# Performance work log

Measured on AMD Instinct MI355X. Metric: run time of the kernel, lower is better.

## Reference

```python
import jax, jax.numpy as jnp
import numpy as np

H = 512   # hidden_size
E = 256   # embedding_size
V = 32000 # vocab_size
L = 1024  # max_length (encoder seq len)
B = 64    # batch


def setup_inputs() -> dict:
    key = jax.random.key(0)
    ks = jax.random.split(key, 18)
    n = lambda i, shape, s=0.05: (jax.random.normal(ks[i], shape, dtype=jnp.float32) * s)
    return {
        "input": jax.random.randint(ks[0], (B, 1), 0, V),
        "last_output_context": n(1, (1, B, H), 1.0),
        "last_hidden": n(2, (1, B, H), 1.0),
        "last_cell_state": n(3, (1, B, H), 1.0),
        "encoder_outputs": n(4, (L, B, H), 1.0),
        "emb": n(5, (V, E)),
        "W_ih": n(6, (4 * H, E + H)),
        "W_hh": n(7, (4 * H, H)),
        "b_ih": n(8, (4 * H,)),
        "b_hh": n(9, (4 * H,)),
        "W_attn": n(10, (H, 2 * H)),
        "b_attn": n(11, (H,)),
        "beta": n(12, (H, 1), 1.0),
        "W_oc": n(13, (H, 2 * H)),
        "b_oc": n(14, (H,)),
        "W_out": n(15, (V, H)),
        "b_out": n(16, (V,)),
    }


def reference(input, last_output_context, last_hidden, last_cell_state,
              encoder_outputs, emb, W_ih, W_hh, b_ih, b_hh,
              W_attn, b_attn, beta, W_oc, b_oc, W_out, b_out):
    # embedding lookup: (B,1) -> (B,E)  (permute(1,0,2) then squeeze step dim)
    tok = emb[input[:, 0]]                                   # (B, E)
    x = jnp.concatenate([tok, last_output_context[0]], axis=1)  # (B, E+H)
    # single-step LSTM (PyTorch gate order i, f, g, o)
    gates = x @ W_ih.T + last_hidden[0] @ W_hh.T + b_ih + b_hh  # (B, 4H)
    i_g, f_g, g_g, o_g = jnp.split(gates, 4, axis=1)
    i_g = jax.nn.sigmoid(i_g)
    f_g = jax.nn.sigmoid(f_g)
    g_g = jnp.tanh(g_g)
    o_g = jax.nn.sigmoid(o_g)
    c = f_g * last_cell_state[0] + i_g * g_g                  # (B, H)
    h = o_g * jnp.tanh(c)                                     # (B, H) == rnn_output
    # additive attention, vectorized over the seq_len loop
    h_tiled = jnp.broadcast_to(h[None], (L, B, H))
    cat = jnp.concatenate([h_tiled, encoder_outputs], axis=-1)  # (L, B, 2H)
    energy = jnp.tanh(cat @ W_attn.T + b_attn) @ beta           # (L, B, 1)
    attn_w = jax.nn.softmax(energy[..., 0], axis=0)             # (L, B) softmax over seq
    # context = bmm(attn_weights, encoder_outputs)
    context = jnp.einsum('lb,lbh->bh', attn_w, encoder_outputs)  # (B, H)
    co = jnp.tanh(jnp.concatenate([h, context], axis=1) @ W_oc.T + b_oc)  # (B, H)
    output = jax.nn.log_softmax(co @ W_out.T + b_out, axis=1)    # (B, V)
    return output, co[None], h[None], c[None]
```

## Files before the change

### kernel.cpp

```cpp
#include <hip/hip_runtime.h>
#include <hip/hip_bf16.h>
#include <cstddef>

#define H   512
#define E   256
#define V   32000
#define L   1024
#define B   64
#define KX  768
#define G2  2048
#define M_TOT 65536

typedef __attribute__((ext_vector_type(8))) _Float16 half8v;
typedef __attribute__((ext_vector_type(4))) float f32x4;

__device__ __forceinline__ half8v cvt8(float4 x0, float4 x1) {
    union { half8v v; _Float16 u[8]; } hv;
    hv.u[0] = (_Float16)x0.x; hv.u[1] = (_Float16)x0.y;
    hv.u[2] = (_Float16)x0.z; hv.u[3] = (_Float16)x0.w;
    hv.u[4] = (_Float16)x1.x; hv.u[5] = (_Float16)x1.y;
    hv.u[6] = (_Float16)x1.z; hv.u[7] = (_Float16)x1.w;
    return hv.v;
}

__device__ __forceinline__ void glds16(const void* g, void* l) {
    __builtin_amdgcn_global_load_lds(
        (const __attribute__((address_space(1))) void*)g,
        (__attribute__((address_space(3))) void*)l, 16, 0, 0);
}

__global__ __launch_bounds__(256) void k_prep(const float* __restrict__ W_attn,
                                              unsigned short* __restrict__ WfB,
                                              const int* __restrict__ inp,
                                              const float* __restrict__ loc,
                                              const float* __restrict__ hprev,
                                              const float* __restrict__ emb,
                                              float* __restrict__ xprevT,
                                              float* __restrict__ xprev_rm) {
    if (blockIdx.x < 128) {
        int u = blockIdx.x * 256 + threadIdx.x;
        int lane = u & 63;
        int rest = u >> 6;
        int f = rest & 7;
        int kt = (rest >> 3) & 15;
        int jt = rest >> 7;
        int wn = f >> 2, nf = f & 3;
        int j = jt * 128 + wn * 64 + nf * 16 + (lane & 15);
        int col = kt * 32 + (lane >> 4) * 8;
        const float* src = &W_attn[(size_t)j * (2 * H) + H + col];
        float4 x0 = *reinterpret_cast<const float4*>(src);
        float4 x1 = *reinterpret_cast<const float4*>(src + 4);
        *reinterpret_cast<half8v*>(&WfB[(size_t)u * 8]) = cvt8(x0, x1);
    } else {
        int gid = (blockIdx.x - 128) * 256 + threadIdx.x;
        int k = gid >> 6, b = gid & 63;
        float v;
        if (k < 256)      v = emb[(size_t)inp[b] * E + k];
        else if (k < 768) v = loc[b * H + (k - 256)];
        else              v = hprev[b * H + (k - 768)];
        xprevT[gid] = v;
        xprev_rm[b * 1280 + k] = v;
    }
}

__global__ __launch_bounds__(256) void k_lstm_mfma(const float* __restrict__ xprev_rm,
                                                   const float* __restrict__ W_ih,
                                                   const float* __restrict__ W_hh,
                                                   const float* __restrict__ b_ih,
                                                   const float* __restrict__ b_hh,
                                                   float* __restrict__ gates) {
    const int tid  = threadIdx.x;
    const int lane = tid & 63;
    const int w    = tid >> 6;
    const int fr   = lane & 15;
    const int kb   = (lane >> 4) * 8;
    const int j    = blockIdx.x * 64 + w * 16 + fr;

    f32x4 acc[4];
    #pragma unroll
    for (int mf = 0; mf < 4; ++mf) acc[mf] = (f32x4){0.f, 0.f, 0.f, 0.f};

    const float* Arow = xprev_rm + (size_t)fr * 1280 + kb;
    const float* Brow1 = W_ih + (size_t)j * KX + kb;
    for (int k0 = 0; k0 < KX; k0 += 32) {
        float4 b0 = *reinterpret_cast<const float4*>(Brow1 + k0);
        float4 b1 = *reinterpret_cast<const float4*>(Brow1 + k0 + 4);
        half8v bh = cvt8(b0, b1);
        #pragma unroll
        for (int mf = 0; mf < 4; ++mf) {
            const float* ap = Arow + (size_t)mf * 16 * 1280 + k0;
            float4 a0 = *reinterpret_cast<const float4*>(ap);
            float4 a1 = *reinterpret_cast<const float4*>(ap + 4);
            acc[mf] = __builtin_amdgcn_mfma_f32_16x16x32_f16(
                cvt8(a0, a1), bh, acc[mf], 0, 0, 0);
        }
    }
    const float* Brow2 = W_hh + (size_t)j * H + kb;
    for (int k0 = 0; k0 < H; k0 += 32) {
        float4 b0 = *reinterpret_cast<const float4*>(Brow2 + k0);
        float4 b1 = *reinterpret_cast<const float4*>(Brow2 + k0 + 4);
        half8v bh = cvt8(b0, b1);
        #pragma unroll
        for (int mf = 0; mf < 4; ++mf) {
            const float* ap = Arow + (size_t)mf * 16 * 1280 + KX + k0;
            float4 a0 = *reinterpret_cast<const float4*>(ap);
            float4 a1 = *reinterpret_cast<const float4*>(ap + 4);
            acc[mf] = __builtin_amdgcn_mfma_f32_16x16x32_f16(
                cvt8(a0, a1), bh, acc[mf], 0, 0, 0);
        }
    }
    float bo = b_ih[j] + b_hh[j];
    #pragma unroll
    for (int mf = 0; mf < 4; ++mf) {
        int mbase = mf * 16 + (lane >> 4) * 4;
        #pragma unroll
        for (int r = 0; r < 4; ++r)
            gates[(size_t)(mbase + r) * G2 + j] = acc[mf][r] + bo;
    }
}

__global__ __launch_bounds__(256) void k_lstm_ep(const float* __restrict__ gates,
                                                 const float* __restrict__ cprev,
                                                 float* __restrict__ h_out,
                                                 float* __restrict__ c_out,
                                                 float* __restrict__ hnewT) {
    int gid = blockIdx.x * 256 + threadIdx.x;
    int b = gid >> 9, u = gid & 511;
    const float* gr = &gates[(size_t)b * G2];
    float ig = 1.f / (1.f + __expf(-gr[u]));
    float fg = 1.f / (1.f + __expf(-gr[u + 512]));
    float gg = tanhf(gr[u + 1024]);
    float og = 1.f / (1.f + __expf(-gr[u + 1536]));
    float c = fg * cprev[b * H + u] + ig * gg;
    float h = og * tanhf(c);
    c_out[b * H + u] = c;
    h_out[b * H + u] = h;
    hnewT[u * 64 + b] = h;
}

__global__ __launch_bounds__(256) void k_hw(const float* __restrict__ W_attn,
                                            const float* __restrict__ b_attn,
                                            const float* __restrict__ hT,
                                            float* __restrict__ hW_jb) {
    int j = blockIdx.x * 4 + (threadIdx.x >> 6);
    int b = threadIdx.x & 63;
    float a0 = 0.f, a1 = 0.f, a2 = 0.f, a3 = 0.f;
    const float* Wr = &W_attn[(size_t)j * (2 * H)];
    for (int k = 0; k < H; k += 4) {
        float4 wv = *reinterpret_cast<const float4*>(&Wr[k]);
        a0 += wv.x * hT[(k + 0) * 64 + b];
        a1 += wv.y * hT[(k + 1) * 64 + b];
        a2 += wv.z * hT[(k + 2) * 64 + b];
        a3 += wv.w * hT[(k + 3) * 64 + b];
    }
    hW_jb[j * 64 + b] = b_attn[j] + ((a0 + a1) + (a2 + a3));
}

__global__ __launch_bounds__(256, 4) void k_energy_v12(
        const float* __restrict__ enc,
        const unsigned short* __restrict__ WfB,
        const float* __restrict__ hW,
        const float* __restrict__ beta,
        float* __restrict__ partial_e) {
    __shared__ float Af[4096];
    __shared__ unsigned short Bh2[4096];
    __shared__ float red[2][128];

    const int tid  = threadIdx.x;
    const int lane = tid & 63;
    const int w    = tid >> 6;
    const int wm = w >> 1;
    const int wn = w & 1;
    const int bid = blockIdx.x;
    const int xcd = bid & 7;
    const int loc = bid >> 3;
    const int mt  = xcd * 64 + (loc >> 2);
    const int jt  = loc & 3;
    const int m0 = mt * 128;
    const int j0 = jt * 128;

    const int fr = lane & 15;
    const int g  = lane >> 4;

    const float* asrcA[4];
    #pragma unroll
    for (int i = 0; i < 4; ++i) {
        int c0 = (w * 4 + i) * 64 + lane;
        int row = c0 >> 3;
        int sc = (lane & 7) ^ (row & 7);
        asrcA[i] = enc + (size_t)(m0 + row) * H + sc * 4;
    }
    const size_t bbase = (size_t)jt * 16 * 512;

    f32x4 acc[4][4];
    #pragma unroll
    for (int i = 0; i < 4; ++i)
        #pragma unroll
        for (int j = 0; j < 4; ++j) acc[i][j] = (f32x4){0.f, 0.f, 0.f, 0.f};

    for (int kt = 0; kt < 16; ++kt) {
        #pragma unroll
        for (int i = 0; i < 4; ++i)
            glds16(asrcA[i] + kt * 32, &Af[((w * 4 + i) * 64 + lane) * 4]);
        #pragma unroll
        for (int i = 0; i < 2; ++i)
            glds16(WfB + (bbase + (size_t)kt * 512 + (w * 2 + i) * 64 + lane) * 8,
                   &Bh2[((w * 2 + i) * 64 + lane) * 8]);
        __syncthreads();
        half8v a_h[4], b_h[4];
        #pragma unroll
        for (int mf = 0; mf < 4; ++mf) {
            int R = wm * 64 + mf * 16 + fr;
            int p0 = (2 * g) ^ (R & 7);
            int p1 = p0 ^ 1;
            float4 f0 = *reinterpret_cast<const float4*>(&Af[(R * 8 + p0) * 4]);
            float4 f1 = *reinterpret_cast<const float4*>(&Af[(R * 8 + p1) * 4]);
            a_h[mf] = cvt8(f0, f1);
        }
        #pragma unroll
        for (int nf = 0; nf < 4; ++nf)
            b_h[nf] = *reinterpret_cast<const half8v*>(
                &Bh2[((wn * 4 + nf) * 64 + lane) * 8]);
        #pragma unroll
        for (int mf = 0; mf < 4; ++mf)
            #pragma unroll
            for (int nf = 0; nf < 4; ++nf)
                acc[mf][nf] = __builtin_amdgcn_mfma_f32_16x16x32_f16(
                    a_h[mf], b_h[nf], acc[mf][nf], 0, 0, 0);
        __syncthreads();
    }

    float psum[4][4];
    #pragma unroll
    for (int i = 0; i < 4; ++i)
        #pragma unroll
        for (int r = 0; r < 4; ++r) psum[i][r] = 0.f;
    #pragma unroll
    for (int nf = 0; nf < 4; ++nf) {
        int jj = j0 + wn * 64 + nf * 16 + (lane & 15);
        float bet = beta[jj];
        #pragma unroll
        for (int mf = 0; mf < 4; ++mf) {
            int b_base = (wm * 64 + mf * 16 + (lane >> 4) * 4) & 63;
            float4 hw4 = *reinterpret_cast<const float4*>(&hW[jj * 64 + b_base]);
            float hwv[4] = {hw4.x, hw4.y, hw4.z, hw4.w};
            #pragma unroll
            for (int r = 0; r < 4; ++r) {
                float e = acc[mf][nf][r] + hwv[r];
                float ex = __expf(2.f * e);
                psum[mf][r] += bet * (1.f - 2.f / (ex + 1.f));
            }
        }
    }
    #pragma unroll
    for (int mf = 0; mf < 4; ++mf)
        #pragma unroll
        for (int r = 0; r < 4; ++r) {
            float v = psum[mf][r];
            v += __shfl_xor(v, 1);
            v += __shfl_xor(v, 2);
            v += __shfl_xor(v, 4);
            v += __shfl_xor(v, 8);
            psum[mf][r] = v;
        }
    __syncthreads();
    if ((lane & 15) == 0) {
        #pragma unroll
        for (int mf = 0; mf < 4; ++mf)
            #pragma unroll
            for (int r = 0; r < 4; ++r)
                red[wn][wm * 64 + mf * 16 + (lane >> 4) * 4 + r] = psum[mf][r];
    }
    __syncthreads();
    if (tid < 128)
        partial_e[(size_t)jt * M_TOT + m0 + tid] = red[0][tid] + red[1][tid];
}

__global__ __launch_bounds__(256) void k_softmax_l(const float* __restrict__ partial_e,
                                                   float* __restrict__ attn_w) {
    int b = blockIdx.x;
    int tid = threadIdx.x;
    float el[4];
    float m = -1e30f;
    #pragma unroll
    for (int i = 0; i < 4; ++i) {
        int l = i * 256 + tid;
        float e = 0.f;
        #pragma unroll
        for (int nb = 0; nb < 4; ++nb)
            e += partial_e[(size_t)nb * M_TOT + l * 64 + b];
        el[i] = e;
        m = fmaxf(m, e);
    }
    #pragma unroll
    for (int s = 1; s < 64; s <<= 1) m = fmaxf(m, __shfl_xor(m, s));
    __shared__ float redm[4];
    if ((tid & 63) == 0) redm[tid >> 6] = m;
    __syncthreads();
    m = fmaxf(fmaxf(redm[0], redm[1]), fmaxf(redm[2], redm[3]));
    float s = 0.f;
    #pragma unroll
    for (int i = 0; i < 4; ++i) { el[i] = __expf(el[i] - m); s += el[i]; }
    #pragma unroll
    for (int sh = 1; sh < 64; sh <<= 1) s += __shfl_xor(s, sh);
    __shared__ float reds[4];
    if ((tid & 63) == 0) reds[tid >> 6] = s;
    __syncthreads();
    s = reds[0] + reds[1] + reds[2] + reds[3];
    float inv = 1.f / s;
    #pragma unroll
    for (int i = 0; i < 4; ++i)
        attn_w[(i * 256 + tid) * 64 + b] = el[i] * inv;
}

__global__ __launch_bounds__(128) void k_ctx_part(const float* __restrict__ attn_w,
                                                  const float* __restrict__ enc,
                                                  float* __restrict__ ctx_part) {
    int chunk = blockIdx.x, b = blockIdx.y;
    int h = threadIdx.x * 4;
    float4 acc = {0.f, 0.f, 0.f, 0.f};
    for (int i = 0; i < 32; ++i) {
        int l = chunk * 32 + i;
        float w = attn_w[l * 64 + b];
        float4 e4 = *reinterpret_cast<const float4*>(
            &enc[((size_t)l * 64 + b) * H + h]);
        acc.x += w * e4.x;
        acc.y += w * e4.y;
        acc.z += w * e4.z;
        acc.w += w * e4.w;
    }
    *reinterpret_cast<float4*>(&ctx_part[((size_t)(chunk * 64 + b)) * H + h]) = acc;
}

__global__ __launch_bounds__(256) void k_ctx_reduce(const float* __restrict__ ctx_part,
                                                    float* __restrict__ ctxT) {
    int gid = blockIdx.x * 256 + threadIdx.x;
    int b = gid >> 9, h = gid & 511;
    float s = 0.f;
    for (int c = 0; c < 32; ++c)
        s += ctx_part[((size_t)(c * 64 + b)) * H + h];
    ctxT[h * 64 + b] = s;
}

__global__ __launch_bounds__(256) void k_co(const float* __restrict__ W_oc,
                                            const float* __restrict__ b_oc,
                                            const float* __restrict__ hT,
                                            const float* __restrict__ ctxT,
                                            float* __restrict__ co_out) {
    int j = blockIdx.x * 4 + (threadIdx.x >> 6);
    int b = threadIdx.x & 63;
    float a0 = 0.f, a1 = 0.f, a2 = 0.f, a3 = 0.f;
    const float* Wr = &W_oc[(size_t)j * (2 * H)];
    for (int k = 0; k < H; k += 4) {
        float4 wv = *reinterpret_cast<const float4*>(&Wr[k]);
        a0 += wv.x * hT[(k + 0) * 64 + b];
        a1 += wv.y * hT[(k + 1) * 64 + b];
        a2 += wv.z * hT[(k + 2) * 64 + b];
        a3 += wv.w * hT[(k + 3) * 64 + b];
    }
    const float* Wr2 = Wr + H;
    for (int k = 0; k < H; k += 4) {
        float4 wv = *reinterpret_cast<const float4*>(&Wr2[k]);
        a0 += wv.x * ctxT[(k + 0) * 64 + b];
        a1 += wv.y * ctxT[(k + 1) * 64 + b];
        a2 += wv.z * ctxT[(k + 2) * 64 + b];
        a3 += wv.w * ctxT[(k + 3) * 64 + b];
    }
    co_out[b * H + j] = tanhf(b_oc[j] + ((a0 + a1) + (a2 + a3)));
}

__global__ __launch_bounds__(256) void k_logits_v3(const float* __restrict__ co,
                                                   const float* __restrict__ W_out,
                                                   const float* __restrict__ b_out,
                                                   float* __restrict__ logits) {
    const int tid  = threadIdx.x;
    const int lane = tid & 63;
    const int w    = tid >> 6;
    const int fr   = lane & 15;
    const int kb   = (lane >> 4) * 8;
    const int j    = blockIdx.x * 64 + w * 16 + fr;

    f32x4 acc[4];
    #pragma unroll
    for (int mf = 0; mf < 4; ++mf) acc[mf] = (f32x4){0.f, 0.f, 0.f, 0.f};

    const float* Arow = &co[(size_t)fr * H + kb];
    const float* Brow = &W_out[(size_t)j * H + kb];

    for (int k0 = 0; k0 < H; k0 += 32) {
        float4 b0 = *reinterpret_cast<const float4*>(Brow + k0);
        float4 b1 = *reinterpret_cast<const float4*>(Brow + k0 + 4);
        half8v bh = cvt8(b0, b1);
        #pragma unroll
        for (int mf = 0; mf < 4; ++mf) {
            const float* ap = Arow + (size_t)mf * 16 * H + k0;
            float4 a0 = *reinterpret_cast<const float4*>(ap);
            float4 a1 = *reinterpret_cast<const float4*>(ap + 4);
            half8v ah = cvt8(a0, a1);
            acc[mf] = __builtin_amdgcn_mfma_f32_16x16x32_f16(ah, bh, acc[mf], 0, 0, 0);
        }
    }
    float bo = b_out[j];
    #pragma unroll
    for (int mf = 0; mf < 4; ++mf) {
        int mbase = mf * 16 + (lane >> 4) * 4;
        #pragma unroll
        for (int r = 0; r < 4; ++r)
            logits[(size_t)(mbase + r) * V + j] = acc[mf][r] + bo;
    }
}

__global__ __launch_bounds__(256) void k_lsm_part(const float* __restrict__ logits,
                                                  float* __restrict__ pmax,
                                                  float* __restrict__ psum) {
    int chunk = blockIdx.x, b = blockIdx.y;
    int tid = threadIdx.x;
    const float* row = &logits[(size_t)b * V + chunk * 4000];
    float v[16];
    float m = -1e30f;
    #pragma unroll
    for (int t = 0; t < 16; ++t) {
        int i = t * 256 + tid;
        v[t] = (i < 4000) ? row[i] : -1e30f;
        m = fmaxf(m, v[t]);
    }
    #pragma unroll
    for (int s = 1; s < 64; s <<= 1) m = fmaxf(m, __shfl_xor(m, s));
    __shared__ float redm[4];
    if ((tid & 63) == 0) redm[tid >> 6] = m;
    __syncthreads();
    m = fmaxf(fmaxf(redm[0], redm[1]), fmaxf(redm[2], redm[3]));
    float s = 0.f;
    #pragma unroll
    for (int t = 0; t < 16; ++t) s += __expf(v[t] - m);
    #pragma unroll
    for (int sh = 1; sh < 64; sh <<= 1) s += __shfl_xor(s, sh);
    __shared__ float reds[4];
    if ((tid & 63) == 0) reds[tid >> 6] = s;
    __syncthreads();
    if (tid == 0) {
        pmax[chunk * 64 + b] = m;
        psum[chunk * 64 + b] = reds[0] + reds[1] + reds[2] + reds[3];
    }
}

__global__ __launch_bounds__(256) void k_lsm_write(const float* __restrict__ logits,
                                                   const float* __restrict__ pmax,
                                                   const float* __restrict__ psum,
                                                   float* __restrict__ out) {
    size_t i4 = ((size_t)blockIdx.x * 256 + threadIdx.x) * 4;
    int b = (int)(i4 / V);
    float m = -1e30f;
    #pragma unroll
    for (int c = 0; c < 8; ++c) m = fmaxf(m, pmax[c * 64 + b]);
    float s = 0.f;
    #pragma unroll
    for (int c = 0; c < 8; ++c) s += psum[c * 64 + b] * __expf(pmax[c * 64 + b] - m);
    float l = m + __logf(s);
    float4 x = *reinterpret_cast<const float4*>(&logits[i4]);
    x.x -= l; x.y -= l; x.z -= l; x.w -= l;
    *reinterpret_cast<float4*>(&out[i4]) = x;
}

extern "C" void kernel_launch(void* const* d_in, const int* in_sizes, int n_in,
                              void* d_out, int out_size, void* d_ws, size_t ws_size,
                              hipStream_t stream) {
    const int*   inp    = (const int*)  d_in[0];
    const float* loc    = (const float*)d_in[1];
    const float* hprev  = (const float*)d_in[2];
    const float* cprev  = (const float*)d_in[3];
    const float* enc    = (const float*)d_in[4];
    const float* emb    = (const float*)d_in[5];
    const float* W_ih   = (const float*)d_in[6];
    const float* W_hh   = (const float*)d_in[7];
    const float* b_ih   = (const float*)d_in[8];
    const float* b_hh   = (const float*)d_in[9];
    const float* W_attn = (const float*)d_in[10];
    const float* b_attn = (const float*)d_in[11];
    const float* beta   = (const float*)d_in[12];
    const float* W_oc   = (const float*)d_in[13];
    const float* b_oc   = (const float*)d_in[14];
    const float* W_out  = (const float*)d_in[15];
    const float* b_out  = (const float*)d_in[16];

    float* out = (float*)d_out;
    float* out_co = out + (size_t)B * V;
    float* out_h  = out_co + B * H;
    float* out_c  = out_h  + B * H;

    float* ws = (float*)d_ws;
    float* xprevT  = ws;
    float* xprev_rm = xprevT + 1280 * 64;
    float* hnewT   = xprev_rm + 1280 * 64;
    float* hW      = hnewT  + H * 64;
    float* gates   = hW     + H * 64;
    float* pe      = gates  + B * G2;
    float* attnw   = pe     + 4 * M_TOT;
    float* ctxp    = attnw  + M_TOT;
    float* ctxT    = ctxp   + 32 * 64 * H;
    float* logits  = ctxT   + H * 64;
    float* pmax    = logits + (size_t)B * V;
    float* psum    = pmax   + 512;
    unsigned short* WfB = (unsigned short*)(psum + 512);

    k_prep  <<<448, 256, 0, stream>>>(W_attn, WfB, inp, loc, hprev, emb,
                                      xprevT, xprev_rm);
    k_lstm_mfma<<<32, 256, 0, stream>>>(xprev_rm, W_ih, W_hh, b_ih, b_hh, gates);
    k_lstm_ep<<<128, 256, 0, stream>>>(gates, cprev, out_h, out_c, hnewT);
    k_hw    <<<128, 256, 0, stream>>>(W_attn, b_attn, hnewT, hW);
    k_energy_v12<<<2048, 256, 0, stream>>>(enc, WfB, hW, beta, pe);
    k_softmax_l<<<64, 256, 0, stream>>>(pe, attnw);
    k_ctx_part <<<dim3(32, 64), 128, 0, stream>>>(attnw, enc, ctxp);
    k_ctx_reduce<<<128, 256, 0, stream>>>(ctxp, ctxT);
    k_co    <<<128, 256, 0, stream>>>(W_oc, b_oc, hnewT, ctxT, out_co);
    k_logits_v3<<<500, 256, 0, stream>>>(out_co, W_out, b_out, logits);
    k_lsm_part<<<dim3(8, 64), 256, 0, stream>>>(logits, pmax, psum);
    k_lsm_write<<<2000, 256, 0, stream>>>(logits, pmax, psum, out);
}
```

Before: 259.4 us.

## Fuse LSTM gate epilogue into MFMA gate kernel and drop unused transpose buffer

Result: no change. 263.7 us (+1.6%).

```diff
diff --git a/kernel.cpp b/kernel.cpp
--- a/kernel.cpp
+++ b/kernel.cpp
@@ -35,7 +35,6 @@
                                               const float* __restrict__ loc,
                                               const float* __restrict__ hprev,
                                               const float* __restrict__ emb,
-                                              float* __restrict__ xprevT,
                                               float* __restrict__ xprev_rm) {
     if (blockIdx.x < 128) {
         int u = blockIdx.x * 256 + threadIdx.x;
@@ -58,23 +57,28 @@
         if (k < 256)      v = emb[(size_t)inp[b] * E + k];
         else if (k < 768) v = loc[b * H + (k - 256)];
         else              v = hprev[b * H + (k - 768)];
-        xprevT[gid] = v;
         xprev_rm[b * 1280 + k] = v;
     }
 }
 
-__global__ __launch_bounds__(256) void k_lstm_mfma(const float* __restrict__ xprev_rm,
-                                                   const float* __restrict__ W_ih,
-                                                   const float* __restrict__ W_hh,
-                                                   const float* __restrict__ b_ih,
-                                                   const float* __restrict__ b_hh,
-                                                   float* __restrict__ gates) {
+__global__ __launch_bounds__(256) void k_lstm_f(const float* __restrict__ xprev_rm,
+                                                const float* __restrict__ W_ih,
+                                                const float* __restrict__ W_hh,
+                                                const float* __restrict__ b_ih,
+                                                const float* __restrict__ b_hh,
+                                                const float* __restrict__ cprev,
+                                                float* __restrict__ h_out,
+                                                float* __restrict__ c_out,
+                                                float* __restrict__ hnewT) {
+    __shared__ float gl[4 * 16 * 64];
+
     const int tid  = threadIdx.x;
     const int lane = tid & 63;
     const int w    = tid >> 6;
     const int fr   = lane & 15;
     const int kb   = (lane >> 4) * 8;
-    const int j    = blockIdx.x * 64 + w * 16 + fr;
+    const int u0   = blockIdx.x * 16;
+    const int j    = w * 512 + u0 + fr;
 
     f32x4 acc[4];
     #pragma unroll
@@ -112,30 +116,27 @@
     float bo = b_ih[j] + b_hh[j];
     #pragma unroll
     for (int mf = 0; mf < 4; ++mf) {
-        int mbase = mf * 16 + (lane >> 4) * 4;
+        int bbase = mf * 16 + (lane >> 4) * 4;
         #pragma unroll
         for (int r = 0; r < 4; ++r)
-            gates[(size_t)(mbase + r) * G2 + j] = acc[mf][r] + bo;
-    }
-}
-
-__global__ __launch_bounds__(256) void k_lstm_ep(const float* __restrict__ gates,
-                                                 const float* __restrict__ cprev,
-                                                 float* __restrict__ h_out,
-                                                 float* __restrict__ c_out,
-                                                 float* __restrict__ hnewT) {
-    int gid = blockIdx.x * 256 + threadIdx.x;
-    int b = gid >> 9, u = gid & 511;
-    const float* gr = &gates[(size_t)b * G2];
-    float ig = 1.f / (1.f + __expf(-gr[u]));
-    float fg = 1.f / (1.f + __expf(-gr[u + 512]));
-    float gg = tanhf(gr[u + 1024]);
-    float og = 1.f / (1.f + __expf(-gr[u + 1536]));
-    float c = fg * cprev[b * H + u] + ig * gg;
-    float h = og * tanhf(c);
-    c_out[b * H + u] = c;
-    h_out[b * H + u] = h;
-    hnewT[u * 64 + b] = h;
+            gl[(w * 16 + fr) * 64 + bbase + r] = acc[mf][r] + bo;
+    }
+    __syncthreads();
+    #pragma unroll
+    for (int i = 0; i < 4; ++i) {
+        int idx = tid * 4 + i;
+        int b = idx & 63, uu = idx >> 6;
+        int u = u0 + uu;
+        float ig = 1.f / (1.f + __expf(-gl[(0 * 16 + uu) * 64 + b]));
+        float fg = 1.f / (1.f + __expf(-gl[(1 * 16 + uu) * 64 + b]));
+        float gg = tanhf(gl[(2 * 16 + uu) * 64 + b]);
+        float og = 1.f / (1.f + __expf(-gl[(3 * 16 + uu) * 64 + b]));
+        float c = fg * cprev[b * H + u] + ig * gg;
+        float h = og * tanhf(c);
+        c_out[b * H + u] = c;
+        h_out[b * H + u] = h;
+        hnewT[u * 64 + b] = h;
+    }
 }
 
 __global__ __launch_bounds__(256) void k_hw(const float* __restrict__ W_attn,
@@ -489,12 +490,10 @@
     float* out_c  = out_h  + B * H;
 
     float* ws = (float*)d_ws;
-    float* xprevT  = ws;
-    float* xprev_rm = xprevT + 1280 * 64;
+    float* xprev_rm = ws;
     float* hnewT   = xprev_rm + 1280 * 64;
     float* hW      = hnewT  + H * 64;
-    float* gates   = hW     + H * 64;
-    float* pe      = gates  + B * G2;
+    float* pe      = hW     + H * 64;
     float* attnw   = pe     + 4 * M_TOT;
     float* ctxp    = attnw  + M_TOT;
     float* ctxT    = ctxp   + 32 * 64 * H;
@@ -503,10 +502,9 @@
     float* psum    = pmax   + 512;
     unsigned short* WfB = (unsigned short*)(psum + 512);
 
-    k_prep  <<<448, 256, 0, stream>>>(W_attn, WfB, inp, loc, hprev, emb,
-                                      xprevT, xprev_rm);
-    k_lstm_mfma<<<32, 256, 0, stream>>>(xprev_rm, W_ih, W_hh, b_ih, b_hh, gates);
-    k_lstm_ep<<<128, 256, 0, stream>>>(gates, cprev, out_h, out_c, hnewT);
+    k_prep  <<<448, 256, 0, stream>>>(W_attn, WfB, inp, loc, hprev, emb, xprev_rm);
+    k_lstm_f<<<32, 256, 0, stream>>>(xprev_rm, W_ih, W_hh, b_ih, b_hh, cprev,
+                                     out_h, out_c, hnewT);
     k_hw    <<<128, 256, 0, stream>>>(W_attn, b_attn, hnewT, hW);
     k_energy_v12<<<2048, 256, 0, stream>>>(enc, WfB, hW, beta, pe);
     k_softmax_l<<<64, 256, 0, stream>>>(pe, attnw);
```
